# Optimization experiments

Measured on AMD Instinct MI355X. Metric: run time of the kernel, lower is better.

The kernel has to match this reference:

```python
import jax, jax.numpy as jnp
import numpy as np

B, NB, S, D = 4096, 16, 256, 1024


def setup_inputs() -> dict:
    key = jax.random.key(0)
    k = jax.random.split(key, 6)
    sc_in = 1.0 / np.sqrt(D)
    sc_out = 1.0 / np.sqrt(S)
    return {
        "x": jax.random.normal(k[0], (B, D), dtype=jnp.float32),
        "y_index": jax.random.randint(k[1], (B, 1), 0, NB, dtype=jnp.int64),
        "W_in": jax.random.uniform(k[2], (NB, S, D), jnp.float32, -sc_in, sc_in),
        "b_in": jax.random.uniform(k[3], (NB, S), jnp.float32, -sc_in, sc_in),
        "W_out": jax.random.uniform(k[4], (NB, D, S), jnp.float32, -sc_out, sc_out),
        "b_out": jax.random.uniform(k[5], (NB, D), jnp.float32, -sc_out, sc_out),
    }


def reference(x, y_index, W_in, b_in, W_out, b_out):
    # h: [B, D] -> relu applied before every branch's fc_in (as in torch source)
    h = jax.nn.relu(x)
    # hiddens for all branches: [B, NB, S]
    hid = jnp.einsum("bd,nsd->bns", h, W_in) + b_in[None, :, :]
    # branch outputs stacked: [B, NB, D]
    outs = jnp.einsum("bns,nds->bnd", hid, W_out) + b_out[None, :, :]
    # gather selected branch per token: [B, D]
    sel = jnp.take_along_axis(outs, y_index[:, :, None], axis=1)[:, 0, :]
    return x + sel
```

## Files before the change

### kernel.cpp

```cpp
#include <hip/hip_runtime.h>


typedef unsigned short u16;
typedef short bf16x8 __attribute__((ext_vector_type(8)));
typedef float f32x4 __attribute__((ext_vector_type(4)));

#define MFMA16 __builtin_amdgcn_mfma_f32_16x16x32_bf16

constexpr int B_TOK = 4096;
constexpr int NB = 16;
constexpr int S_DIM = 256;
constexpr int D_DIM = 1024;
constexpr int BM = 64;
constexpr int PAD_ROWS = B_TOK + NB * BM;
constexpr int NTILES = PAD_ROWS / BM;

__device__ __forceinline__ unsigned short f2bf(float f) {
    unsigned u = __builtin_bit_cast(unsigned, f);
    u += 0x7fffu + ((u >> 16) & 1u);
    return (unsigned short)(u >> 16);
}
__device__ __forceinline__ unsigned pack2(float a, float b) {
    return (unsigned)f2bf(a) | ((unsigned)f2bf(b) << 16);
}

__device__ __forceinline__ void gload_lds16(const void* g, void* l) {
    __builtin_amdgcn_global_load_lds(
        (const __attribute__((address_space(1))) void*)g,
        (__attribute__((address_space(3))) void*)l, 16, 0, 0);
}

__global__ __launch_bounds__(256) void setup_kernel(
    const int* __restrict__ y, int* __restrict__ perm, int* __restrict__ tileBranch) {
    __shared__ int hist[NB];
    __shared__ int aoff[NB + 1];
    __shared__ int cursor[NB];
    const int t = threadIdx.x;
    if (t < NB) hist[t] = 0;
    __syncthreads();
    for (int i = t; i < B_TOK; i += 256) atomicAdd(&hist[y[i]], 1);
    __syncthreads();
    if (t == 0) {
        int off = 0;
        for (int n = 0; n < NB; ++n) {
            aoff[n] = off;
            cursor[n] = off;
            off += ((hist[n] + BM - 1) / BM) * BM;
        }
        aoff[NB] = off;
    }
    __syncthreads();
    for (int i = t; i < NTILES; i += 256) {
        int rb = i * BM, br = -1;
        for (int n = 0; n < NB; ++n)
            if (rb >= aoff[n] && rb < aoff[n + 1]) br = n;
        tileBranch[i] = br;
    }
    for (int i = t; i < PAD_ROWS; i += 256) perm[i] = -1;
    __syncthreads();
    for (int i = t; i < B_TOK; i += 256) {
        int n = y[i];
        int pos = atomicAdd(&cursor[n], 1);
        perm[pos] = i;
    }
}

__global__ __launch_bounds__(256) void cast_w(
    const float* __restrict__ src, u16* __restrict__ dst, int n8) {
    int i = blockIdx.x * 256 + threadIdx.x;
    if (i >= n8) return;
    const float4* p = (const float4*)src + (size_t)i * 2;
    float4 v0 = p[0], v1 = p[1];
    uint4 o;
    o.x = pack2(v0.x, v0.y);
    o.y = pack2(v0.z, v0.w);
    o.z = pack2(v1.x, v1.y);
    o.w = pack2(v1.z, v1.w);
    ((uint4*)dst)[i] = o;
}

__global__ __launch_bounds__(256) void cast_x(
    const float* __restrict__ x, const int* __restrict__ perm, u16* __restrict__ Xp) {
    int tid = blockIdx.x * 256 + threadIdx.x;
    int row = tid >> 7;
    int c8 = (tid & 127) << 3;
    int tok = perm[row];
    uint4 o;
    if (tok >= 0) {
        const float4* p = (const float4*)&x[(size_t)tok * D_DIM + c8];
        float4 v0 = p[0], v1 = p[1];
        o.x = pack2(fmaxf(v0.x, 0.f), fmaxf(v0.y, 0.f));
        o.y = pack2(fmaxf(v0.z, 0.f), fmaxf(v0.w, 0.f));
        o.z = pack2(fmaxf(v1.x, 0.f), fmaxf(v1.y, 0.f));
        o.w = pack2(fmaxf(v1.z, 0.f), fmaxf(v1.w, 0.f));
    } else {
        o = make_uint4(0, 0, 0, 0);
    }
    *(uint4*)&Xp[(size_t)row * D_DIM + c8] = o;
}

template <bool FINAL>
__global__ __launch_bounds__(256) void gemm_tile(
    const u16* __restrict__ A, int lda,
    const u16* __restrict__ Bw,
    const float* __restrict__ bias,
    const int* __restrict__ tileBranch,
    const int* __restrict__ perm,
    const float* __restrict__ xres,
    u16* __restrict__ HpOut,
    float* __restrict__ out,
    int K, int N) {
    const int branch = tileBranch[blockIdx.y];
    if (branch < 0) return;
    const int rowBase = blockIdx.y * BM;
    const int colBase = blockIdx.x * 64;

    __shared__ u16 sA[64 * 64];
    __shared__ u16 sB[64 * 64];

    const int t = threadIdx.x;
    const int srow = t >> 3;
    const int scolB = (t & 7) << 4;

    const u16* Bb = Bw + (size_t)branch * N * K + (size_t)colBase * K;

    const int lane = t & 63;
    const int wm = ((t >> 7) & 1) * 32;
    const int wn = ((t >> 6) & 1) * 32;
    const int fr = lane & 15;
    const int kc = (lane >> 4) * 8;

    f32x4 acc[2][2] = {};

    const int nK = K >> 6;
    for (int kt = 0; kt < nK; ++kt) {
        const int k0 = kt << 6;
#pragma unroll
        for (int i = 0; i < 2; ++i) {
            const char* g = (const char*)A +
                (((size_t)(rowBase + srow + i * 32)) * lda + k0) * 2 + scolB;
            gload_lds16(g, &sA[(i * 32 + srow) * 64 + (scolB >> 1)]);
        }
#pragma unroll
        for (int i = 0; i < 2; ++i) {
            const char* g = (const char*)Bb +
                (((size_t)(srow + i * 32)) * K + k0) * 2 + scolB;
            gload_lds16(g, &sB[(i * 32 + srow) * 64 + (scolB >> 1)]);
        }
        __syncthreads();
#pragma unroll
        for (int kk = 0; kk < 2; ++kk) {
            const int kcol = kc + kk * 32;
            bf16x8 a0 = *(const bf16x8*)&sA[(wm + fr) * 64 + kcol];
            bf16x8 a1 = *(const bf16x8*)&sA[(wm + 16 + fr) * 64 + kcol];
            bf16x8 b0 = *(const bf16x8*)&sB[(wn + fr) * 64 + kcol];
            bf16x8 b1 = *(const bf16x8*)&sB[(wn + 16 + fr) * 64 + kcol];
            acc[0][0] = MFMA16(a0, b0, acc[0][0], 0, 0, 0);
            acc[0][1] = MFMA16(a0, b1, acc[0][1], 0, 0, 0);
            acc[1][0] = MFMA16(a1, b0, acc[1][0], 0, 0, 0);
            acc[1][1] = MFMA16(a1, b1, acc[1][1], 0, 0, 0);
        }
        __syncthreads();
    }

    const int r0 = (lane >> 4) * 4;
#pragma unroll
    for (int m = 0; m < 2; ++m) {
        const int prow0 = rowBase + wm + m * 16 + r0;
#pragma unroll
        for (int n = 0; n < 2; ++n) {
            const int col = colBase + wn + n * 16 + fr;
            const float bv = bias[branch * N + col];
#pragma unroll
            for (int r = 0; r < 4; ++r) {
                const float v = acc[m][n][r] + bv;
                const int prow = prow0 + r;
                if constexpr (!FINAL) {
                    HpOut[(size_t)prow * N + col] = f2bf(v);
                } else {
                    const int tok = perm[prow];
                    if (tok >= 0) {
                        const size_t o = (size_t)tok * N + col;
                        out[o] = xres[o] + v;
                    }
                }
            }
        }
    }
}

extern "C" void kernel_launch(void* const* d_in, const int* in_sizes, int n_in,
                              void* d_out, int out_size, void* d_ws, size_t ws_size,
                              hipStream_t stream) {
    const float* x     = (const float*)d_in[0];
    const int*   y     = (const int*)d_in[1];
    const float* W_in  = (const float*)d_in[2];
    const float* b_in  = (const float*)d_in[3];
    const float* W_out = (const float*)d_in[4];
    const float* b_out = (const float*)d_in[5];
    float* out = (float*)d_out;

    char* ws = (char*)d_ws;
    u16* Wi = (u16*)(ws);
    u16* Wo = (u16*)(ws + 8388608);
    u16* Xp = (u16*)(ws + 16777216);
    u16* Hp = (u16*)(ws + 27262976);
    int* perm = (int*)(ws + 29884416);
    int* tileBranch = (int*)(ws + 29904896);

    setup_kernel<<<1, 256, 0, stream>>>(y, perm, tileBranch);

    cast_w<<<2048, 256, 0, stream>>>(W_in, Wi, 4194304 / 8);
    cast_w<<<2048, 256, 0, stream>>>(W_out, Wo, 4194304 / 8);

    cast_x<<<2560, 256, 0, stream>>>(x, perm, Xp);

    gemm_tile<false><<<dim3(S_DIM / 64, NTILES), 256, 0, stream>>>(
        Xp, D_DIM, Wi, b_in, tileBranch, perm,
        nullptr, Hp, nullptr, D_DIM, S_DIM);

    gemm_tile<true><<<dim3(D_DIM / 64, NTILES), 256, 0, stream>>>(
        Hp, S_DIM, Wo, b_out, tileBranch, perm,
        x, nullptr, out, S_DIM, D_DIM);
}
```

Before: 61.88 us.

## Fuse setup and weight casts, fold x cast into GEMM1, widen tiles with swizzled LDS

Merges the routing setup and both weight casts into one launch, with block 0 building the permutation and the other blocks converting weights. The separate relu+bf16 cast of x into a padded buffer is removed: GEMM1 gathers x rows through perm, casts them in registers and writes them to LDS, prefetching the next K slice. Both GEMMs widen the N tile from 64 to 128 and use XOR-swizzled LDS layouts to reduce bank conflicts. This cuts launches and the intermediate Xp round trip, but GEMM1 now runs with only 2 column blocks per row tile, which lowers parallelism for that kernel.

```diff
diff --git a/kernel.cpp b/kernel.cpp
--- a/kernel.cpp
+++ b/kernel.cpp
@@ -23,142 +23,150 @@
 __device__ __forceinline__ unsigned pack2(float a, float b) {
     return (unsigned)f2bf(a) | ((unsigned)f2bf(b) << 16);
 }
-
 __device__ __forceinline__ void gload_lds16(const void* g, void* l) {
     __builtin_amdgcn_global_load_lds(
         (const __attribute__((address_space(1))) void*)g,
         (__attribute__((address_space(3))) void*)l, 16, 0, 0);
 }
 
-__global__ __launch_bounds__(256) void setup_kernel(
+__global__ __launch_bounds__(256) void prep_kernel(
+    const float* __restrict__ Wi_f, const float* __restrict__ Wo_f,
+    u16* __restrict__ Wi, u16* __restrict__ Wo,
     const int* __restrict__ y, int* __restrict__ perm, int* __restrict__ tileBranch) {
-    __shared__ int hist[NB];
-    __shared__ int aoff[NB + 1];
-    __shared__ int cursor[NB];
     const int t = threadIdx.x;
-    if (t < NB) hist[t] = 0;
-    __syncthreads();
-    for (int i = t; i < B_TOK; i += 256) atomicAdd(&hist[y[i]], 1);
-    __syncthreads();
-    if (t == 0) {
-        int off = 0;
-        for (int n = 0; n < NB; ++n) {
-            aoff[n] = off;
-            cursor[n] = off;
-            off += ((hist[n] + BM - 1) / BM) * BM;
-        }
-        aoff[NB] = off;
-    }
-    __syncthreads();
-    for (int i = t; i < NTILES; i += 256) {
-        int rb = i * BM, br = -1;
-        for (int n = 0; n < NB; ++n)
-            if (rb >= aoff[n] && rb < aoff[n + 1]) br = n;
-        tileBranch[i] = br;
-    }
-    for (int i = t; i < PAD_ROWS; i += 256) perm[i] = -1;
-    __syncthreads();
-    for (int i = t; i < B_TOK; i += 256) {
-        int n = y[i];
-        int pos = atomicAdd(&cursor[n], 1);
-        perm[pos] = i;
-    }
-}
-
-__global__ __launch_bounds__(256) void cast_w(
-    const float* __restrict__ src, u16* __restrict__ dst, int n8) {
-    int i = blockIdx.x * 256 + threadIdx.x;
-    if (i >= n8) return;
-    const float4* p = (const float4*)src + (size_t)i * 2;
+    if (blockIdx.x == 0) {
+        __shared__ int hist[NB];
+        __shared__ int aoff[NB + 1];
+        __shared__ int cursor[NB];
+        if (t < NB) hist[t] = 0;
+        __syncthreads();
+        for (int i = t; i < B_TOK; i += 256) atomicAdd(&hist[y[i]], 1);
+        __syncthreads();
+        if (t == 0) {
+            int off = 0;
+            for (int n = 0; n < NB; ++n) {
+                aoff[n] = off;
+                cursor[n] = off;
+                off += ((hist[n] + BM - 1) / BM) * BM;
+            }
+            aoff[NB] = off;
+        }
+        __syncthreads();
+        for (int i = t; i < NTILES; i += 256) {
+            int rb = i * BM, br = -1;
+            for (int n = 0; n < NB; ++n)
+                if (rb >= aoff[n] && rb < aoff[n + 1]) br = n;
+            tileBranch[i] = br;
+        }
+        for (int i = t; i < PAD_ROWS; i += 256) perm[i] = -1;
+        __syncthreads();
+        for (int i = t; i < B_TOK; i += 256) {
+            int pos = atomicAdd(&cursor[y[i]], 1);
+            perm[pos] = i;
+        }
+        return;
+    }
+    int i = (blockIdx.x - 1) * 256 + t;
+    const float* src;
+    u16* dst;
+    int j;
+    if (i < 524288) { src = Wi_f; dst = Wi; j = i; }
+    else            { src = Wo_f; dst = Wo; j = i - 524288; }
+    const float4* p = (const float4*)src + (size_t)j * 2;
     float4 v0 = p[0], v1 = p[1];
     uint4 o;
     o.x = pack2(v0.x, v0.y);
     o.y = pack2(v0.z, v0.w);
     o.z = pack2(v1.x, v1.y);
     o.w = pack2(v1.z, v1.w);
-    ((uint4*)dst)[i] = o;
-}
-
-__global__ __launch_bounds__(256) void cast_x(
-    const float* __restrict__ x, const int* __restrict__ perm, u16* __restrict__ Xp) {
-    int tid = blockIdx.x * 256 + threadIdx.x;
-    int row = tid >> 7;
-    int c8 = (tid & 127) << 3;
-    int tok = perm[row];
-    uint4 o;
-    if (tok >= 0) {
-        const float4* p = (const float4*)&x[(size_t)tok * D_DIM + c8];
-        float4 v0 = p[0], v1 = p[1];
-        o.x = pack2(fmaxf(v0.x, 0.f), fmaxf(v0.y, 0.f));
-        o.y = pack2(fmaxf(v0.z, 0.f), fmaxf(v0.w, 0.f));
-        o.z = pack2(fmaxf(v1.x, 0.f), fmaxf(v1.y, 0.f));
-        o.w = pack2(fmaxf(v1.z, 0.f), fmaxf(v1.w, 0.f));
-    } else {
-        o = make_uint4(0, 0, 0, 0);
-    }
-    *(uint4*)&Xp[(size_t)row * D_DIM + c8] = o;
-}
-
-template <bool FINAL>
-__global__ __launch_bounds__(256) void gemm_tile(
-    const u16* __restrict__ A, int lda,
-    const u16* __restrict__ Bw,
-    const float* __restrict__ bias,
-    const int* __restrict__ tileBranch,
-    const int* __restrict__ perm,
-    const float* __restrict__ xres,
-    u16* __restrict__ HpOut,
-    float* __restrict__ out,
-    int K, int N) {
+    ((uint4*)dst)[j] = o;
+}
+
+__global__ __launch_bounds__(256) void gemm1_kernel(
+    const float* __restrict__ x, const u16* __restrict__ Wi,
+    const float* __restrict__ b_in, const int* __restrict__ tileBranch,
+    const int* __restrict__ perm, u16* __restrict__ Hp) {
     const int branch = tileBranch[blockIdx.y];
     if (branch < 0) return;
     const int rowBase = blockIdx.y * BM;
-    const int colBase = blockIdx.x * 64;
+    const int colBase = blockIdx.x * 128;
 
     __shared__ u16 sA[64 * 64];
-    __shared__ u16 sB[64 * 64];
+    __shared__ u16 sB[128 * 64];
 
     const int t = threadIdx.x;
-    const int srow = t >> 3;
-    const int scolB = (t & 7) << 4;
-
-    const u16* Bb = Bw + (size_t)branch * N * K + (size_t)colBase * K;
+    const int ar = t >> 2;
+    const int acg = t & 3;
+    const int tok = perm[rowBase + ar];
+    const float* aSrc = (tok >= 0) ? (x + (size_t)tok * D_DIM + acg * 16) : x;
+    const int abyte0 = (ar * 128 + acg * 32) ^ ((ar & 7) << 4);
+    const int abyte1 = (ar * 128 + acg * 32 + 16) ^ ((ar & 7) << 4);
+
+    const u16* Bb = Wi + (size_t)branch * S_DIM * D_DIM + (size_t)colBase * D_DIM;
 
     const int lane = t & 63;
-    const int wm = ((t >> 7) & 1) * 32;
-    const int wn = ((t >> 6) & 1) * 32;
+    const int wid = t >> 6;
+    const int wm = (wid >> 1) * 32;
+    const int wn = (wid & 1) * 64;
     const int fr = lane & 15;
-    const int kc = (lane >> 4) * 8;
-
-    f32x4 acc[2][2] = {};
-
-    const int nK = K >> 6;
-    for (int kt = 0; kt < nK; ++kt) {
+    const int kc = (lane >> 4) << 3;
+
+    f32x4 acc[2][4] = {};
+
+    float4 v0, v1, v2, v3;
+    {
+        const float4* p = (const float4*)aSrc;
+        v0 = p[0]; v1 = p[1]; v2 = p[2]; v3 = p[3];
+    }
+
+    for (int kt = 0; kt < 16; ++kt) {
         const int k0 = kt << 6;
 #pragma unroll
-        for (int i = 0; i < 2; ++i) {
-            const char* g = (const char*)A +
-                (((size_t)(rowBase + srow + i * 32)) * lda + k0) * 2 + scolB;
-            gload_lds16(g, &sA[(i * 32 + srow) * 64 + (scolB >> 1)]);
-        }
-#pragma unroll
-        for (int i = 0; i < 2; ++i) {
-            const char* g = (const char*)Bb +
-                (((size_t)(srow + i * 32)) * K + k0) * 2 + scolB;
-            gload_lds16(g, &sB[(i * 32 + srow) * 64 + (scolB >> 1)]);
+        for (int i = 0; i < 4; ++i) {
+            const int L = i * 4096 + t * 16;
+            const int row = L >> 7;
+            const int sunit = ((L >> 4) & 7) ^ (row & 7);
+            const char* g = (const char*)Bb + (size_t)row * (D_DIM * 2) + k0 * 2 + sunit * 16;
+            gload_lds16(g, (char*)sB + L);
+        }
+        uint4 w0, w1;
+        if (tok >= 0) {
+            w0.x = pack2(fmaxf(v0.x, 0.f), fmaxf(v0.y, 0.f));
+            w0.y = pack2(fmaxf(v0.z, 0.f), fmaxf(v0.w, 0.f));
+            w0.z = pack2(fmaxf(v1.x, 0.f), fmaxf(v1.y, 0.f));
+            w0.w = pack2(fmaxf(v1.z, 0.f), fmaxf(v1.w, 0.f));
+            w1.x = pack2(fmaxf(v2.x, 0.f), fmaxf(v2.y, 0.f));
+            w1.y = pack2(fmaxf(v2.z, 0.f), fmaxf(v2.w, 0.f));
+            w1.z = pack2(fmaxf(v3.x, 0.f), fmaxf(v3.y, 0.f));
+            w1.w = pack2(fmaxf(v3.z, 0.f), fmaxf(v3.w, 0.f));
+        } else {
+            w0 = make_uint4(0, 0, 0, 0);
+            w1 = make_uint4(0, 0, 0, 0);
+        }
+        *(uint4*)((char*)sA + abyte0) = w0;
+        *(uint4*)((char*)sA + abyte1) = w1;
+        if (kt < 15) {
+            const float4* p = (const float4*)(aSrc + (k0 + 64));
+            v0 = p[0]; v1 = p[1]; v2 = p[2]; v3 = p[3];
         }
         __syncthreads();
 #pragma unroll
         for (int kk = 0; kk < 2; ++kk) {
             const int kcol = kc + kk * 32;
-            bf16x8 a0 = *(const bf16x8*)&sA[(wm + fr) * 64 + kcol];
-            bf16x8 a1 = *(const bf16x8*)&sA[(wm + 16 + fr) * 64 + kcol];
-            bf16x8 b0 = *(const bf16x8*)&sB[(wn + fr) * 64 + kcol];
-            bf16x8 b1 = *(const bf16x8*)&sB[(wn + 16 + fr) * 64 + kcol];
-            acc[0][0] = MFMA16(a0, b0, acc[0][0], 0, 0, 0);
-            acc[0][1] = MFMA16(a0, b1, acc[0][1], 0, 0, 0);
-            acc[1][0] = MFMA16(a1, b0, acc[1][0], 0, 0, 0);
-            acc[1][1] = MFMA16(a1, b1, acc[1][1], 0, 0, 0);
+            const int ra0 = wm + fr, ra1 = wm + 16 + fr;
+            bf16x8 a0 = *(const bf16x8*)&sA[(ra0 * 64 + kcol) ^ ((ra0 & 7) << 3)];
+            bf16x8 a1 = *(const bf16x8*)&sA[(ra1 * 64 + kcol) ^ ((ra1 & 7) << 3)];
+            bf16x8 b[4];
+#pragma unroll
+            for (int n = 0; n < 4; ++n) {
+                const int rb = wn + n * 16 + fr;
+                b[n] = *(const bf16x8*)&sB[(rb * 64 + kcol) ^ ((rb & 7) << 3)];
+            }
+#pragma unroll
+            for (int n = 0; n < 4; ++n) {
+                acc[0][n] = MFMA16(a0, b[n], acc[0][n], 0, 0, 0);
+                acc[1][n] = MFMA16(a1, b[n], acc[1][n], 0, 0, 0);
+            }
         }
         __syncthreads();
     }
@@ -168,22 +176,95 @@
     for (int m = 0; m < 2; ++m) {
         const int prow0 = rowBase + wm + m * 16 + r0;
 #pragma unroll
-        for (int n = 0; n < 2; ++n) {
+        for (int n = 0; n < 4; ++n) {
             const int col = colBase + wn + n * 16 + fr;
-            const float bv = bias[branch * N + col];
-#pragma unroll
-            for (int r = 0; r < 4; ++r) {
-                const float v = acc[m][n][r] + bv;
-                const int prow = prow0 + r;
-                if constexpr (!FINAL) {
-                    HpOut[(size_t)prow * N + col] = f2bf(v);
-                } else {
-                    const int tok = perm[prow];
-                    if (tok >= 0) {
-                        const size_t o = (size_t)tok * N + col;
-                        out[o] = xres[o] + v;
-                    }
-                }
+            const float bv = b_in[branch * S_DIM + col];
+#pragma unroll
+            for (int r = 0; r < 4; ++r)
+                Hp[(size_t)(prow0 + r) * S_DIM + col] = f2bf(acc[m][n][r] + bv);
+        }
+    }
+}
+
+__global__ __launch_bounds__(256) void gemm2_kernel(
+    const u16* __restrict__ Hp, const u16* __restrict__ Wo,
+    const float* __restrict__ b_out, const int* __restrict__ tileBranch,
+    const int* __restrict__ perm, const float* __restrict__ x,
+    float* __restrict__ out) {
+    const int branch = tileBranch[blockIdx.y];
+    if (branch < 0) return;
+    const int rowBase = blockIdx.y * BM;
+    const int colBase = blockIdx.x * 128;
+
+    __shared__ u16 sA[64 * 64];
+    __shared__ u16 sB[128 * 64];
+
+    const int t = threadIdx.x;
+    const u16* Ab = Hp + (size_t)rowBase * S_DIM;
+    const u16* Bb = Wo + (size_t)branch * D_DIM * S_DIM + (size_t)colBase * S_DIM;
+
+    const int lane = t & 63;
+    const int wid = t >> 6;
+    const int wm = (wid >> 1) * 32;
+    const int wn = (wid & 1) * 64;
+    const int fr = lane & 15;
+    const int kc = (lane >> 4) << 3;
+
+    f32x4 acc[2][4] = {};
+
+    for (int kt = 0; kt < 4; ++kt) {
+        const int k0 = kt << 6;
+#pragma unroll
+        for (int i = 0; i < 2; ++i) {
+            const int L = i * 4096 + t * 16;
+            const int row = L >> 7;
+            const int sunit = ((L >> 4) & 7) ^ (row & 7);
+            const char* g = (const char*)Ab + (size_t)row * (S_DIM * 2) + k0 * 2 + sunit * 16;
+            gload_lds16(g, (char*)sA + L);
+        }
+#pragma unroll
+        for (int i = 0; i < 4; ++i) {
+            const int L = i * 4096 + t * 16;
+            const int row = L >> 7;
+            const int sunit = ((L >> 4) & 7) ^ (row & 7);
+            const char* g = (const char*)Bb + (size_t)row * (S_DIM * 2) + k0 * 2 + sunit * 16;
+            gload_lds16(g, (char*)sB + L);
+        }
+        __syncthreads();
+#pragma unroll
+        for (int kk = 0; kk < 2; ++kk) {
+            const int kcol = kc + kk * 32;
+            const int ra0 = wm + fr, ra1 = wm + 16 + fr;
+            bf16x8 a0 = *(const bf16x8*)&sA[(ra0 * 64 + kcol) ^ ((ra0 & 7) << 3)];
+            bf16x8 a1 = *(const bf16x8*)&sA[(ra1 * 64 + kcol) ^ ((ra1 & 7) << 3)];
+            bf16x8 b[4];
+#pragma unroll
+            for (int n = 0; n < 4; ++n) {
+                const int rb = wn + n * 16 + fr;
+                b[n] = *(const bf16x8*)&sB[(rb * 64 + kcol) ^ ((rb & 7) << 3)];
+            }
+#pragma unroll
+            for (int n = 0; n < 4; ++n) {
+                acc[0][n] = MFMA16(a0, b[n], acc[0][n], 0, 0, 0);
+                acc[1][n] = MFMA16(a1, b[n], acc[1][n], 0, 0, 0);
+            }
+        }
+        __syncthreads();
+    }
+
+    const int r0 = (lane >> 4) * 4;
+#pragma unroll
+    for (int m = 0; m < 2; ++m) {
+        const int prow0 = rowBase + wm + m * 16 + r0;
+#pragma unroll
+        for (int r = 0; r < 4; ++r) {
+            const int tok = perm[prow0 + r];
+            if (tok < 0) continue;
+#pragma unroll
+            for (int n = 0; n < 4; ++n) {
+                const int col = colBase + wn + n * 16 + fr;
+                const size_t o = (size_t)tok * D_DIM + col;
+                out[o] = x[o] + acc[m][n][r] + b_out[branch * D_DIM + col];
             }
         }
     }
@@ -203,23 +284,15 @@
     char* ws = (char*)d_ws;
     u16* Wi = (u16*)(ws);
     u16* Wo = (u16*)(ws + 8388608);
-    u16* Xp = (u16*)(ws + 16777216);
-    u16* Hp = (u16*)(ws + 27262976);
-    int* perm = (int*)(ws + 29884416);
-    int* tileBranch = (int*)(ws + 29904896);
-
-    setup_kernel<<<1, 256, 0, stream>>>(y, perm, tileBranch);
-
-    cast_w<<<2048, 256, 0, stream>>>(W_in, Wi, 4194304 / 8);
-    cast_w<<<2048, 256, 0, stream>>>(W_out, Wo, 4194304 / 8);
-
-    cast_x<<<2560, 256, 0, stream>>>(x, perm, Xp);
-
-    gemm_tile<false><<<dim3(S_DIM / 64, NTILES), 256, 0, stream>>>(
-        Xp, D_DIM, Wi, b_in, tileBranch, perm,
-        nullptr, Hp, nullptr, D_DIM, S_DIM);
-
-    gemm_tile<true><<<dim3(D_DIM / 64, NTILES), 256, 0, stream>>>(
-        Hp, S_DIM, Wo, b_out, tileBranch, perm,
-        x, nullptr, out, S_DIM, D_DIM);
-}
+    u16* Hp = (u16*)(ws + 16777216);
+    int* perm = (int*)(ws + 19398656);
+    int* tileBranch = (int*)(ws + 19419136);
+
+    prep_kernel<<<4097, 256, 0, stream>>>(W_in, W_out, Wi, Wo, y, perm, tileBranch);
+
+    gemm1_kernel<<<dim3(S_DIM / 128, NTILES), 256, 0, stream>>>(
+        x, Wi, b_in, tileBranch, perm, Hp);
+
+    gemm2_kernel<<<dim3(D_DIM / 128, NTILES), 256, 0, stream>>>(
+        Hp, Wo, b_out, tileBranch, perm, x, out);
+}
```

New measurement: 57.32 us. 7.4% less time.
